# Kernel tuning notes

Hardware: AMD Instinct MI355X
Metric: run time of the kernel (lower is better)

## Reference

```python
import jax, jax.numpy as jnp
from jax import lax
import numpy as np

B, P, ENC, DEC, ATT, E, S, V = 32, 196, 512, 512, 512, 256, 128, 10000

def setup_inputs() -> dict:
    key = jax.random.key(0)
    ks = jax.random.split(key, 20)
    g = lambda k, shape, s=0.02: jax.random.normal(k, shape, dtype=jnp.float32) * s
    return {
        'features': jax.random.normal(ks[0], (B, P, ENC), dtype=jnp.float32),
        'captions': jax.random.randint(ks[1], (B, S), 0, V, dtype=jnp.int64),
        'emb': g(ks[2], (V, E)),
        'W_enc_att': g(ks[3], (ENC, ATT)), 'b_enc_att': jnp.zeros((ATT,), jnp.float32),
        'W_dec_att': g(ks[4], (DEC, ATT)), 'b_dec_att': jnp.zeros((ATT,), jnp.float32),
        'v_att': g(ks[5], (ATT,)), 'b_full_att': jnp.zeros((), jnp.float32),
        'W_init_h': g(ks[6], (ENC, DEC)), 'b_init_h': jnp.zeros((DEC,), jnp.float32),
        'W_init_c': g(ks[7], (ENC, DEC)), 'b_init_c': jnp.zeros((DEC,), jnp.float32),
        'W_ih': g(ks[8], (4 * DEC, E + ENC)), 'W_hh': g(ks[9], (4 * DEC, DEC)),
        'b_ih': jnp.zeros((4 * DEC,), jnp.float32), 'b_hh': jnp.zeros((4 * DEC,), jnp.float32),
        'W_fcn': g(ks[10], (DEC, V)), 'b_fcn': jnp.zeros((V,), jnp.float32),
    }

def reference(features, captions, emb, W_enc_att, b_enc_att, W_dec_att, b_dec_att,
              v_att, b_full_att, W_init_h, b_init_h, W_init_c, b_init_c,
              W_ih, W_hh, b_ih, b_hh, W_fcn, b_fcn):
    # init hidden state from mean encoder features
    mean_f = features.mean(axis=1)                    # [B, ENC]
    h = mean_f @ W_init_h + b_init_h                  # [B, DEC]
    c = mean_f @ W_init_c + b_init_c
    embeds = emb[captions]                            # [B, S, E]
    feat_proj = features @ W_enc_att + b_enc_att      # [B, P, ATT], loop-invariant

    def step(carry, emb_t):
        h, c = carry
        # additive attention: tanh(Uf + Wh) . v -> softmax -> weighted sum
        att = jnp.tanh(feat_proj + (h @ W_dec_att + b_dec_att)[:, None, :])  # [B, P, ATT]
        scores = att @ v_att + b_full_att             # [B, P]
        alpha = jax.nn.softmax(scores, axis=1)
        context = jnp.einsum('bp,bpe->be', alpha, features)  # [B, ENC]
        x = jnp.concatenate([emb_t, context], axis=1)  # [B, E+ENC]
        gates = x @ W_ih.T + b_ih + h @ W_hh.T + b_hh  # [B, 4*DEC]
        i, f, g, o = jnp.split(gates, 4, axis=1)
        c_new = jax.nn.sigmoid(f) * c + jax.nn.sigmoid(i) * jnp.tanh(g)
        h_new = jax.nn.sigmoid(o) * jnp.tanh(c_new)
        out = h_new @ W_fcn + b_fcn                    # dropout = identity (eval)
        return (h_new, c_new), out

    xs = jnp.swapaxes(embeds[:, :S - 1], 0, 1)         # [S-1, B, E]
    _, preds = lax.scan(step, (h, c), xs)              # [S-1, B, V]
    return jnp.swapaxes(preds, 0, 1)                   # [B, S-1, V]
```

## Files before the change

kernel.cpp:

```cpp
#include <hip/hip_runtime.h>
#include <hip/hip_bf16.h>
#include <stdint.h>

#define BB 32
#define PP 196
#define ENC 512
#define DEC 512
#define ATTD 512
#define EE 256
#define SS 128
#define VV 10000
#define TT 127
#define NBLK 512

typedef unsigned short ushort_t;
typedef unsigned int uint_t;
typedef unsigned long long u64_t;
typedef float f32x4 __attribute__((ext_vector_type(4)));
typedef short s16x8 __attribute__((ext_vector_type(8)));

__device__ __forceinline__ float bf2f(ushort_t u) {
    uint_t x = ((uint_t)u) << 16;
    return __uint_as_float(x);
}
__device__ __forceinline__ float bflo(uint_t u) { return __uint_as_float(u << 16); }
__device__ __forceinline__ float bfhi(uint_t u) { return __uint_as_float(u & 0xffff0000u); }
__device__ __forceinline__ ushort_t f2bf(float f) {
    uint_t u = __float_as_uint(f);
    uint_t r = (u + 0x7FFFu + ((u >> 16) & 1u)) >> 16;
    return (ushort_t)r;
}
__device__ __forceinline__ float ftanh(float x) {
    x = fminf(15.f, fmaxf(-15.f, x));
    float e = __expf(2.f * x);
    return (e - 1.f) * __builtin_amdgcn_rcpf(e + 1.f);
}
__device__ __forceinline__ float fsig(float x) {
    return __builtin_amdgcn_rcpf(1.f + __expf(-x));
}

__device__ __forceinline__ float aload1(const float* p) {
    return __hip_atomic_load(p, __ATOMIC_RELAXED, __HIP_MEMORY_SCOPE_AGENT);
}
__device__ __forceinline__ void astore1(float* p, float v) {
    __hip_atomic_store(p, v, __ATOMIC_RELAXED, __HIP_MEMORY_SCOPE_AGENT);
}
__device__ __forceinline__ float2 aload2(const float* p) {
    u64_t v = __hip_atomic_load((const u64_t*)p, __ATOMIC_RELAXED, __HIP_MEMORY_SCOPE_AGENT);
    float2 r;
    r.x = __uint_as_float((uint_t)v);
    r.y = __uint_as_float((uint_t)(v >> 32));
    return r;
}


__global__ void k_cvt(const float* __restrict__ s, ushort_t* __restrict__ d, int n) {
    for (int i = blockIdx.x * blockDim.x + threadIdx.x; i < n; i += gridDim.x * blockDim.x)
        d[i] = f2bf(s[i]);
}

__global__ void k_cvtD(const float* __restrict__ Wdec, ushort_t* __restrict__ out) {
    const int n = DEC * ATTD;
    for (int i = blockIdx.x * blockDim.x + threadIdx.x; i < n; i += gridDim.x * blockDim.x) {
        int k = i & (ATTD - 1);
        int j = i >> 9;
        out[i] = f2bf(Wdec[(size_t)k * ATTD + j]);
    }
}

__global__ void k_embed_bf(const int* __restrict__ cap, const float* __restrict__ emb,
                           ushort_t* __restrict__ out) {
    const int n = TT * BB * EE;
    for (int i = blockIdx.x * blockDim.x + threadIdx.x; i < n; i += gridDim.x * blockDim.x) {
        int e = i & (EE - 1);
        int b = (i >> 8) & (BB - 1);
        int t = i >> 13;
        int tok = cap[b * SS + t];
        out[i] = f2bf(emb[(size_t)tok * EE + e]);
    }
}

__global__ void k_cvtT(const float* __restrict__ Wih, ushort_t* __restrict__ out) {
    const int n = EE * 4 * DEC;
    for (int i = blockIdx.x * blockDim.x + threadIdx.x; i < n; i += gridDim.x * blockDim.x) {
        int k = i & (EE - 1);
        int row = i >> 8;
        out[(size_t)k * (4 * DEC) + row] = f2bf(Wih[(size_t)row * (EE + ENC) + k]);
    }
}

__global__ void k_cvtG2(const float* __restrict__ Wih, const float* __restrict__ Whh,
                        ushort_t* __restrict__ out) {
    const int n = 16 * 2 * 64 * 128 * 8;
    for (int i = blockIdx.x * blockDim.x + threadIdx.x; i < n; i += gridDim.x * blockDim.x) {
        int j = i & 7;
        int R = (i >> 3) & 127;
        int kc = (i >> 10) & 63;
        int kh = (i >> 16) & 1;
        int pcg = i >> 17;
        int d = pcg * 32 + (R >> 2);
        int gate = R & 3;
        int row = gate * DEC + d;
        int k = kh * 512 + kc * 8 + j;
        float v = (k < 512) ? Wih[(size_t)row * (EE + ENC) + EE + k]
                            : Whh[(size_t)row * DEC + (k - 512)];
        out[i] = f2bf(v);
    }
}

__global__ void k_bsum(const float* __restrict__ a, const float* __restrict__ b,
                       float* __restrict__ o, int n) {
    int i = blockIdx.x * blockDim.x + threadIdx.x;
    if (i < n) o[i] = a[i] + b[i];
}

__global__ __launch_bounds__(256) void k_init(const float* __restrict__ feat,
                                              const float* __restrict__ Wh, const float* __restrict__ bh,
                                              const float* __restrict__ Wc, const float* __restrict__ bc,
                                              float* __restrict__ h0, float* __restrict__ c0,
                                              int* __restrict__ bar) {
    __shared__ float ms[ENC];
    int b = blockIdx.x, t = threadIdx.x;
    if (b == 0) {
        for (int i = t; i < 4096; i += 256) bar[i] = 0;
    }
    for (int c = t; c < ENC; c += 256) {
        float s = 0.f;
        for (int p = 0; p < PP; ++p) s += feat[((size_t)b * PP + p) * ENC + c];
        ms[c] = s * (1.f / (float)PP);
    }
    __syncthreads();
    int d0 = 2 * t;
    float ah0 = 0.f, ah1 = 0.f, ac0 = 0.f, ac1 = 0.f;
    for (int k = 0; k < ENC; ++k) {
        float mk = ms[k];
        float2 wh = *(const float2*)(Wh + (size_t)k * DEC + d0);
        float2 wc = *(const float2*)(Wc + (size_t)k * DEC + d0);
        ah0 += mk * wh.x; ah1 += mk * wh.y;
        ac0 += mk * wc.x; ac1 += mk * wc.y;
    }
    h0[b * DEC + d0] = ah0 + bh[d0];
    h0[b * DEC + d0 + 1] = ah1 + bh[d0 + 1];
    c0[b * DEC + d0] = ac0 + bc[d0];
    c0[b * DEC + d0 + 1] = ac1 + bc[d0 + 1];
}

template <int MODE>
__global__ __launch_bounds__(256) void k_gemm(const ushort_t* __restrict__ A,
                                              const ushort_t* __restrict__ Bm,
                                              const float* __restrict__ bias,
                                              ushort_t* __restrict__ outb,
                                              float* __restrict__ outf,
                                              int M, int N, int K) {
    __shared__ __align__(16) ushort_t As[128 * 32];
    __shared__ __align__(16) ushort_t Bs[128 * 32];

    const int tid = threadIdx.x;
    const int wid = tid >> 6, lane = tid & 63;
    const int wm = wid >> 1, wn = wid & 1;
    const int lr = lane & 15, lk = (lane >> 4) * 8;
    const int row0 = blockIdx.x * 128, col0 = blockIdx.y * 128;

    f32x4 acc[4][4];
#pragma unroll
    for (int i = 0; i < 4; ++i)
#pragma unroll
        for (int j = 0; j < 4; ++j) acc[i][j] = (f32x4){0.f, 0.f, 0.f, 0.f};

    for (int k0 = 0; k0 < K; k0 += 32) {
        {
            int r = tid >> 1, kk = (tid & 1) * 16;
            int gr = row0 + r;
            uint4 v0 = {0, 0, 0, 0}, v1 = {0, 0, 0, 0};
            if (gr < M) {
                const ushort_t* sp = A + (size_t)gr * K + k0 + kk;
                v0 = *(const uint4*)sp;
                v1 = *(const uint4*)(sp + 8);
            }
            *(uint4*)(As + r * 32 + kk) = v0;
            *(uint4*)(As + r * 32 + kk + 8) = v1;
        }
        {
            int kk = tid >> 3;
            int n = (tid & 7) * 16;
            const ushort_t* sp = Bm + (size_t)(k0 + kk) * N + col0 + n;
            ushort_t tmp[16];
            if (col0 + n + 16 <= N) {
                *(uint4*)tmp = *(const uint4*)sp;
                *(uint4*)(tmp + 8) = *(const uint4*)(sp + 8);
            } else {
#pragma unroll
                for (int j = 0; j < 16; ++j) {
                    int c = col0 + n + j;
                    tmp[j] = (c < N) ? sp[j] : (ushort_t)0;
                }
            }
#pragma unroll
            for (int j = 0; j < 16; ++j) Bs[(n + j) * 32 + kk] = tmp[j];
        }
        __syncthreads();
        s16x8 af[4], bfr[4];
#pragma unroll
        for (int i = 0; i < 4; ++i)
            af[i] = *(const s16x8*)(As + (wm * 64 + i * 16 + lr) * 32 + lk);
#pragma unroll
        for (int j = 0; j < 4; ++j)
            bfr[j] = *(const s16x8*)(Bs + (wn * 64 + j * 16 + lr) * 32 + lk);
#pragma unroll
        for (int i = 0; i < 4; ++i)
#pragma unroll
            for (int j = 0; j < 4; ++j)
                acc[i][j] = __builtin_amdgcn_mfma_f32_16x16x32_bf16(af[i], bfr[j], acc[i][j], 0, 0, 0);
        __syncthreads();
    }

    const int lrow = (lane >> 4) * 4;
#pragma unroll
    for (int i = 0; i < 4; ++i) {
#pragma unroll
        for (int j = 0; j < 4; ++j) {
            int gr0 = row0 + wm * 64 + i * 16 + lrow;
            int gc = col0 + wn * 64 + j * 16 + lr;
#pragma unroll
            for (int r = 0; r < 4; ++r) {
                int gr = gr0 + r;
                if (gr < M && gc < N) {
                    float v = acc[i][j][r] + bias[gc];
                    if (MODE == 0) {
                        outb[(size_t)gr * N + gc] = f2bf(v);
                    } else {
                        int t = gr >> 5, b = gr & 31;
                        outf[((size_t)(b * TT + t)) * VV + gc] = v;
                    }
                }
            }
        }
    }
}


__device__ __forceinline__ void gbar16(int* cnt, int target) {
    asm volatile("s_waitcnt vmcnt(0)" ::: "memory");
    __syncthreads();
    if (threadIdx.x == 0) {
        __hip_atomic_fetch_add(cnt, 1, __ATOMIC_RELAXED, __HIP_MEMORY_SCOPE_AGENT);
        while (__hip_atomic_load(cnt, __ATOMIC_RELAXED, __HIP_MEMORY_SCOPE_AGENT) < target)
            __builtin_amdgcn_s_sleep(1);
    }
    __syncthreads();
}

__global__ __launch_bounds__(256) void k_steps(
    const ushort_t* __restrict__ fp, const ushort_t* __restrict__ fb,
    const ushort_t* __restrict__ WdecT, const float* __restrict__ bdec,
    const float* __restrict__ vatt, const float* __restrict__ bfull,
    const ushort_t* __restrict__ Wg2, const ushort_t* __restrict__ gemb,
    float* __restrict__ hbuf, const float* __restrict__ cbuf,
    float* __restrict__ a_glob, float* __restrict__ ctxP, float* __restrict__ Sp,
    ushort_t* __restrict__ Hb, int* __restrict__ bar) {

    __shared__ __align__(16) float hs[8 * 68];
    __shared__ __align__(16) float asS[544];
    __shared__ __align__(16) float vsS[544];
    __shared__ __align__(16) float cs[512];
    __shared__ __align__(16) float pctx[4 * 520];
    __shared__ float ep[16];
    __shared__ float sS[1];

    const int bid = blockIdx.x, tid = threadIdx.x;
    const float bfull_r = bfull[0];

    const int q = bid & 7, r = bid >> 3;
    const int pcg = 2 * q + (r & 1);
    const int bA = r >> 1;
    int* grpcnt = bar + 576 + bA * 32;

    const int aj = tid >> 3, akh = tid & 7;
    const int j_abs = pcg * 32 + aj;
    const float bdec_r = bdec[j_abs];
    const int pl = tid >> 4, ks = tid & 15;
    const int cnt_b = (pcg < 4) ? 13 : 12;
    const int p0 = (pcg < 4) ? pcg * 13 : 52 + (pcg - 4) * 12;
    const int ps = tid >> 6, cg = tid & 63;
    const int R = tid >> 1, ckh = tid & 1;
    const int cd = pcg * 32 + (R >> 2);
    const int crow = (R & 3) * DEC + cd;
    const ushort_t* wgp = Wg2 + ((size_t)(pcg * 2 + ckh) * 64) * 1024 + R * 8;

    float creg = ((tid & 7) == 0) ? cbuf[bA * DEC + cd] : 0.f;

    {
        int k0 = tid, k1 = tid + 256;
        vsS[(k0 & 31) + (k0 >> 5) * 34] = vatt[k0];
        vsS[(k1 & 31) + (k1 >> 5) * 34] = vatt[k1];
    }
    __syncthreads();

    for (int st = 0; st < TT; ++st) {
        const float* h_in = hbuf + (size_t)(st & 1) * BB * DEC;
        float* h_out = hbuf + (size_t)((st + 1) & 1) * BB * DEC;
        const size_t trow = (size_t)st * BB + bA;

        {
            float2 hv = aload2(h_in + bA * DEC + 2 * tid);
            int k0 = 2 * tid;
            float* hrow = hs + (k0 >> 6) * 68 + (k0 & 63);
            hrow[0] = hv.x;
            hrow[1] = hv.y;
        }
        __syncthreads();
        {
            const ushort_t* wp = WdecT + (size_t)j_abs * 512 + akh * 64;
            const float* hp = hs + akh * 68;
            float acc = 0.f;
#pragma unroll
            for (int c = 0; c < 8; ++c) {
                uint4 wv = *(const uint4*)(wp + c * 8);
                f32x4 x0 = *(const f32x4*)(hp + c * 8);
                f32x4 x1 = *(const f32x4*)(hp + c * 8 + 4);
                acc += bflo(wv.x) * x0[0] + bfhi(wv.x) * x0[1]
                     + bflo(wv.y) * x0[2] + bfhi(wv.y) * x0[3]
                     + bflo(wv.z) * x1[0] + bfhi(wv.z) * x1[1]
                     + bflo(wv.w) * x1[2] + bfhi(wv.w) * x1[3];
            }
            acc += __shfl_xor(acc, 1);
            acc += __shfl_xor(acc, 2);
            acc += __shfl_xor(acc, 4);
            if (akh == 0) astore1(a_glob + bA * ATTD + j_abs, acc + bdec_r);
        }
        gbar16(grpcnt, 16 * (3 * st + 1));

        {
            float2 av = aload2(a_glob + bA * ATTD + 2 * tid);
            int k0 = 2 * tid;
            float* arow = asS + (k0 & 31) + (k0 >> 5) * 34;
            arow[0] = av.x;
            arow[1] = av.y;
        }
        __syncthreads();
        {
            float acc = 0.f;
            if (pl < cnt_b) {
                const int p = p0 + pl;
                const ushort_t* fr = fp + ((size_t)bA * PP + p) * ATTD + ks * 32;
                const float* ap = asS + ks * 34;
                const float* vp = vsS + ks * 34;
#pragma unroll
                for (int c2 = 0; c2 < 4; ++c2) {
                    uint4 fv = *(const uint4*)(fr + c2 * 8);
                    const int c = c2 * 8;
                    float2 a0 = *(const float2*)(ap + c),     a1 = *(const float2*)(ap + c + 2);
                    float2 a2 = *(const float2*)(ap + c + 4), a3 = *(const float2*)(ap + c + 6);
                    float2 v0 = *(const float2*)(vp + c),     v1 = *(const float2*)(vp + c + 2);
                    float2 v2 = *(const float2*)(vp + c + 4), v3 = *(const float2*)(vp + c + 6);
                    acc += ftanh(bflo(fv.x) + a0.x) * v0.x;
                    acc += ftanh(bfhi(fv.x) + a0.y) * v0.y;
                    acc += ftanh(bflo(fv.y) + a1.x) * v1.x;
                    acc += ftanh(bfhi(fv.y) + a1.y) * v1.y;
                    acc += ftanh(bflo(fv.z) + a2.x) * v2.x;
                    acc += ftanh(bfhi(fv.z) + a2.y) * v2.y;
                    acc += ftanh(bflo(fv.w) + a3.x) * v3.x;
                    acc += ftanh(bfhi(fv.w) + a3.y) * v3.y;
                }
            }
            acc += __shfl_xor(acc, 1);
            acc += __shfl_xor(acc, 2);
            acc += __shfl_xor(acc, 4);
            acc += __shfl_xor(acc, 8);
            if (ks == 0) ep[pl] = (pl < cnt_b) ? __expf(acc + bfull_r) : 0.f;
        }
        __syncthreads();
        if (tid < 16) {
            float v = ep[tid];
            v += __shfl_xor(v, 1);
            v += __shfl_xor(v, 2);
            v += __shfl_xor(v, 4);
            v += __shfl_xor(v, 8);
            if (tid == 0) astore1(Sp + bA * 16 + pcg, v);
        }
        {
            float a8[8];
#pragma unroll
            for (int i2 = 0; i2 < 8; ++i2) a8[i2] = 0.f;
            for (int p2 = ps; p2 < cnt_b; p2 += 4) {
                float e2 = ep[p2];
                uint4 fv = *(const uint4*)(fb + ((size_t)bA * PP + p0 + p2) * ENC + cg * 8);
                a8[0] += e2 * bflo(fv.x); a8[1] += e2 * bfhi(fv.x);
                a8[2] += e2 * bflo(fv.y); a8[3] += e2 * bfhi(fv.y);
                a8[4] += e2 * bflo(fv.z); a8[5] += e2 * bfhi(fv.z);
                a8[6] += e2 * bflo(fv.w); a8[7] += e2 * bfhi(fv.w);
            }
            float* pp = pctx + ps * 520 + cg * 8;
            *(f32x4*)pp = (f32x4){a8[0], a8[1], a8[2], a8[3]};
            *(f32x4*)(pp + 4) = (f32x4){a8[4], a8[5], a8[6], a8[7]};
        }
        __syncthreads();
        {
            int c0i = 2 * tid, c1i = 2 * tid + 1;
            float s0 = pctx[c0i] + pctx[520 + c0i] + pctx[1040 + c0i] + pctx[1560 + c0i];
            float s1 = pctx[c1i] + pctx[520 + c1i] + pctx[1040 + c1i] + pctx[1560 + c1i];
            float* cp = ctxP + ((size_t)bA * 16 + pcg) * 512;
            astore1(cp + c0i, s0);
            astore1(cp + c1i, s1);
        }
        gbar16(grpcnt, 16 * (3 * st + 2));

        {
            if (tid < 16) {
                float s = aload1(Sp + bA * 16 + tid);
                s += __shfl_xor(s, 1);
                s += __shfl_xor(s, 2);
                s += __shfl_xor(s, 4);
                s += __shfl_xor(s, 8);
                if (tid == 0) sS[0] = s;
            }
            __syncthreads();
            const float invS = __builtin_amdgcn_rcpf(sS[0]);
            float s0 = 0.f, s1 = 0.f;
            const float* cp = ctxP + (size_t)bA * 16 * 512 + 2 * tid;
#pragma unroll
            for (int sl = 0; sl < 16; ++sl) {
                float2 v = aload2(cp + sl * 512);
                s0 += v.x;
                s1 += v.y;
            }
            cs[2 * tid] = s0 * invS;
            cs[2 * tid + 1] = s1 * invS;
        }
        __syncthreads();
        {
            float acc0 = 0.f, acc1 = 0.f;
#pragma unroll 8
            for (int kc = 0; kc < 64; ++kc) {
                uint4 wv = *(const uint4*)(wgp + kc * 1024);
                const float* xp = ckh ? (hs + (kc >> 3) * 68 + (kc & 7) * 8) : (cs + kc * 8);
                f32x4 x0 = *(const f32x4*)xp;
                f32x4 x1 = *(const f32x4*)(xp + 4);
                acc0 += bflo(wv.x) * x0[0] + bfhi(wv.x) * x0[1]
                      + bflo(wv.y) * x0[2] + bfhi(wv.y) * x0[3];
                acc1 += bflo(wv.z) * x1[0] + bfhi(wv.z) * x1[1]
                      + bflo(wv.w) * x1[2] + bfhi(wv.w) * x1[3];
            }
            float acc = acc0 + acc1;
            acc += __shfl_xor(acc, 1);
            const size_t gidx = trow * (4 * DEC) + crow;
            acc += bf2f(gemb[gidx]);
            float pf = __shfl_xor(acc, 2);
            float pg = __shfl_xor(acc, 4);
            float po = __shfl_xor(acc, 6);
            if ((tid & 7) == 0) {
                float cn = fsig(pf) * creg + fsig(acc) * ftanh(pg);
                float hn = fsig(po) * ftanh(cn);
                creg = cn;
                astore1(h_out + bA * DEC + cd, hn);
                Hb[trow * DEC + cd] = f2bf(hn);
            }
        }
        gbar16(grpcnt, 16 * (3 * st + 3));
    }
}


extern "C" void kernel_launch(void* const* d_in, const int* in_sizes, int n_in,
                              void* d_out, int out_size, void* d_ws, size_t ws_size,
                              hipStream_t stream) {
    const float* features  = (const float*)d_in[0];
    const int*   captions  = (const int*)d_in[1];
    const float* emb       = (const float*)d_in[2];
    const float* W_enc_att = (const float*)d_in[3];
    const float* b_enc_att = (const float*)d_in[4];
    const float* W_dec_att = (const float*)d_in[5];
    const float* b_dec_att = (const float*)d_in[6];
    const float* v_att     = (const float*)d_in[7];
    const float* b_full    = (const float*)d_in[8];
    const float* W_init_h  = (const float*)d_in[9];
    const float* b_init_h  = (const float*)d_in[10];
    const float* W_init_c  = (const float*)d_in[11];
    const float* b_init_c  = (const float*)d_in[12];
    const float* W_ih      = (const float*)d_in[13];
    const float* W_hh      = (const float*)d_in[14];
    const float* b_ih      = (const float*)d_in[15];
    const float* b_hh      = (const float*)d_in[16];
    const float* W_fcn     = (const float*)d_in[17];
    const float* b_fcn     = (const float*)d_in[18];
    float* out = (float*)d_out;
    char* ws = (char*)d_ws;

    size_t o = 0;
    ushort_t* Wfcn_b  = (ushort_t*)(ws + o); o += (size_t)DEC * VV * 2;
    ushort_t* Wenc_b  = (ushort_t*)(ws + o); o += (size_t)ENC * ATTD * 2;
    ushort_t* WdecT   = (ushort_t*)(ws + o); o += (size_t)DEC * ATTD * 2;
    ushort_t* fb      = (ushort_t*)(ws + o); o += (size_t)BB * PP * ENC * 2;
    ushort_t* fp_b    = (ushort_t*)(ws + o); o += (size_t)BB * PP * ATTD * 2;
    ushort_t* emb_bf  = (ushort_t*)(ws + o); o += (size_t)TT * BB * EE * 2;
    ushort_t* WihT    = (ushort_t*)(ws + o); o += (size_t)EE * 4 * DEC * 2;
    ushort_t* gembuf  = (ushort_t*)(ws + o); o += (size_t)TT * BB * 4 * DEC * 2;
    ushort_t* Wg2     = (ushort_t*)(ws + o); o += (size_t)4 * DEC * 1024 * 2;
    float*    bsum    = (float*)(ws + o);    o += (size_t)4 * DEC * 4;
    ushort_t* Hb      = (ushort_t*)(ws + o); o += (size_t)TT * BB * DEC * 2;
    float*    hbuf    = (float*)(ws + o);    o += (size_t)2 * BB * DEC * 4;
    float*    cbuf    = (float*)(ws + o);    o += (size_t)BB * DEC * 4;
    float*    a_glob  = (float*)(ws + o);    o += (size_t)BB * ATTD * 4;
    float*    ctxP    = (float*)(ws + o);    o += (size_t)BB * 16 * 512 * 4;
    float*    Sp      = (float*)(ws + o);    o += (size_t)BB * 16 * 4 + 64;
    int*      bar     = (int*)(ws + o);      o += 4096 * 4;

    k_cvt<<<2048, 256, 0, stream>>>(W_fcn, Wfcn_b, DEC * VV);
    k_cvt<<<256, 256, 0, stream>>>(W_enc_att, Wenc_b, ENC * ATTD);
    k_cvtD<<<256, 256, 0, stream>>>(W_dec_att, WdecT);
    k_cvt<<<2048, 256, 0, stream>>>(features, fb, BB * PP * ENC);
    k_embed_bf<<<1024, 256, 0, stream>>>(captions, emb, emb_bf);
    k_cvtT<<<1024, 256, 0, stream>>>(W_ih, WihT);
    k_cvtG2<<<4096, 256, 0, stream>>>(W_ih, W_hh, Wg2);
    k_bsum<<<8, 256, 0, stream>>>(b_ih, b_hh, bsum, 4 * DEC);
    k_init<<<32, 256, 0, stream>>>(features, W_init_h, b_init_h, W_init_c, b_init_c,
                                   hbuf, cbuf, bar);
    k_gemm<0><<<dim3((BB * PP) / 128, ATTD / 128), 256, 0, stream>>>(
        fb, Wenc_b, b_enc_att, fp_b, nullptr, BB * PP, ATTD, ENC);
    k_gemm<0><<<dim3((TT * BB + 127) / 128, (4 * DEC) / 128), 256, 0, stream>>>(
        emb_bf, WihT, bsum, gembuf, nullptr, TT * BB, 4 * DEC, EE);

    k_steps<<<NBLK, 256, 0, stream>>>(fp_b, fb, WdecT, b_dec_att, v_att, b_full,
                                      Wg2, gembuf, hbuf, cbuf,
                                      a_glob, ctxP, Sp, Hb, bar);

    k_gemm<1><<<dim3((TT * BB + 127) / 128, (VV + 127) / 128), 256, 0, stream>>>(
        Hb, Wfcn_b, b_fcn, nullptr, out, TT * BB, VV, DEC);
}
```

Baseline: 2.675 ms.

## Fuse decoder attention projection into LSTM update to drop one group barrier per step

Each block now computes a partial of the next step's h@W_dec_att, using the 32 hidden values it has just produced. It writes that partial to a per-slice buffer (paP), which is zero-initialized in k_init. At the start of the next step, the 16 partials are summed along with the bias. This removes the separate attention-projection phase and one of the three inter-block barriers per timestep. In exchange, each step reads 16 partial vectors from global memory, and the workspace grows by the size of the partial buffer.

```diff
diff --git a/kernel.cpp b/kernel.cpp
--- a/kernel.cpp
+++ b/kernel.cpp
@@ -118,12 +118,13 @@
                                               const float* __restrict__ Wh, const float* __restrict__ bh,
                                               const float* __restrict__ Wc, const float* __restrict__ bc,
                                               float* __restrict__ h0, float* __restrict__ c0,
-                                              int* __restrict__ bar) {
+                                              float* __restrict__ paP, int* __restrict__ bar) {
     __shared__ float ms[ENC];
     int b = blockIdx.x, t = threadIdx.x;
     if (b == 0) {
         for (int i = t; i < 4096; i += 256) bar[i] = 0;
     }
+    for (int i = t; i < 16 * 512; i += 256) paP[(size_t)b * 16 * 512 + i] = 0.f;
     for (int c = t; c < ENC; c += 256) {
         float s = 0.f;
         for (int p = 0; p < PP; ++p) s += feat[((size_t)b * PP + p) * ENC + c];
@@ -256,7 +257,7 @@
     const float* __restrict__ vatt, const float* __restrict__ bfull,
     const ushort_t* __restrict__ Wg2, const ushort_t* __restrict__ gemb,
     float* __restrict__ hbuf, const float* __restrict__ cbuf,
-    float* __restrict__ a_glob, float* __restrict__ ctxP, float* __restrict__ Sp,
+    float* __restrict__ paP, float* __restrict__ ctxP, float* __restrict__ Sp,
     ushort_t* __restrict__ Hb, int* __restrict__ bar) {
 
     __shared__ __align__(16) float hs[8 * 68];
@@ -264,6 +265,7 @@
     __shared__ __align__(16) float vsS[544];
     __shared__ __align__(16) float cs[512];
     __shared__ __align__(16) float pctx[4 * 520];
+    __shared__ __align__(16) float hsNew[32];
     __shared__ float ep[16];
     __shared__ float sS[1];
 
@@ -277,7 +279,6 @@
 
     const int aj = tid >> 3, akh = tid & 7;
     const int j_abs = pcg * 32 + aj;
-    const float bdec_r = bdec[j_abs];
     const int pl = tid >> 4, ks = tid & 15;
     const int cnt_b = (pcg < 4) ? 13 : 12;
     const int p0 = (pcg < 4) ? pcg * 13 : 52 + (pcg - 4) * 12;
@@ -286,6 +287,8 @@
     const int cd = pcg * 32 + (R >> 2);
     const int crow = (R & 3) * DEC + cd;
     const ushort_t* wgp = Wg2 + ((size_t)(pcg * 2 + ckh) * 64) * 1024 + R * 8;
+    float* mypa = paP + ((size_t)bA * 16 + pcg) * 512;
+    const float2 bdec2 = *(const float2*)(bdec + 2 * tid);
 
     float creg = ((tid & 7) == 0) ? cbuf[bA * DEC + cd] : 0.f;
 
@@ -296,46 +299,55 @@
     }
     __syncthreads();
 
+    {
+        float2 hv = aload2(hbuf + bA * DEC + 2 * tid);
+        int k0 = 2 * tid;
+        float* hrow = hs + (k0 >> 6) * 68 + (k0 & 63);
+        hrow[0] = hv.x;
+        hrow[1] = hv.y;
+        __syncthreads();
+        const ushort_t* wp = WdecT + (size_t)j_abs * 512 + akh * 64;
+        const float* hp = hs + akh * 68;
+        float acc = 0.f;
+#pragma unroll
+        for (int c = 0; c < 8; ++c) {
+            uint4 wv = *(const uint4*)(wp + c * 8);
+            f32x4 x0 = *(const f32x4*)(hp + c * 8);
+            f32x4 x1 = *(const f32x4*)(hp + c * 8 + 4);
+            acc += bflo(wv.x) * x0[0] + bfhi(wv.x) * x0[1]
+                 + bflo(wv.y) * x0[2] + bfhi(wv.y) * x0[3]
+                 + bflo(wv.z) * x1[0] + bfhi(wv.z) * x1[1]
+                 + bflo(wv.w) * x1[2] + bfhi(wv.w) * x1[3];
+        }
+        acc += __shfl_xor(acc, 1);
+        acc += __shfl_xor(acc, 2);
+        acc += __shfl_xor(acc, 4);
+        if (akh == 0) astore1(mypa + j_abs, acc);
+    }
+    gbar16(grpcnt, 16);
+
     for (int st = 0; st < TT; ++st) {
         const float* h_in = hbuf + (size_t)(st & 1) * BB * DEC;
         float* h_out = hbuf + (size_t)((st + 1) & 1) * BB * DEC;
         const size_t trow = (size_t)st * BB + bA;
 
         {
+            float s0 = bdec2.x, s1 = bdec2.y;
+            const float* pap = paP + (size_t)bA * 16 * 512 + 2 * tid;
+#pragma unroll
+            for (int sl = 0; sl < 16; ++sl) {
+                float2 v = aload2(pap + sl * 512);
+                s0 += v.x;
+                s1 += v.y;
+            }
+            int k0 = 2 * tid;
+            float* arow = asS + (k0 & 31) + (k0 >> 5) * 34;
+            arow[0] = s0;
+            arow[1] = s1;
             float2 hv = aload2(h_in + bA * DEC + 2 * tid);
-            int k0 = 2 * tid;
             float* hrow = hs + (k0 >> 6) * 68 + (k0 & 63);
             hrow[0] = hv.x;
             hrow[1] = hv.y;
-        }
-        __syncthreads();
-        {
-            const ushort_t* wp = WdecT + (size_t)j_abs * 512 + akh * 64;
-            const float* hp = hs + akh * 68;
-            float acc = 0.f;
-#pragma unroll
-            for (int c = 0; c < 8; ++c) {
-                uint4 wv = *(const uint4*)(wp + c * 8);
-                f32x4 x0 = *(const f32x4*)(hp + c * 8);
-                f32x4 x1 = *(const f32x4*)(hp + c * 8 + 4);
-                acc += bflo(wv.x) * x0[0] + bfhi(wv.x) * x0[1]
-                     + bflo(wv.y) * x0[2] + bfhi(wv.y) * x0[3]
-                     + bflo(wv.z) * x1[0] + bfhi(wv.z) * x1[1]
-                     + bflo(wv.w) * x1[2] + bfhi(wv.w) * x1[3];
-            }
-            acc += __shfl_xor(acc, 1);
-            acc += __shfl_xor(acc, 2);
-            acc += __shfl_xor(acc, 4);
-            if (akh == 0) astore1(a_glob + bA * ATTD + j_abs, acc + bdec_r);
-        }
-        gbar16(grpcnt, 16 * (3 * st + 1));
-
-        {
-            float2 av = aload2(a_glob + bA * ATTD + 2 * tid);
-            int k0 = 2 * tid;
-            float* arow = asS + (k0 & 31) + (k0 >> 5) * 34;
-            arow[0] = av.x;
-            arow[1] = av.y;
         }
         __syncthreads();
         {
@@ -403,7 +415,7 @@
             astore1(cp + c0i, s0);
             astore1(cp + c1i, s1);
         }
-        gbar16(grpcnt, 16 * (3 * st + 2));
+        gbar16(grpcnt, 16 * (2 * st + 2));
 
         {
             if (tid < 16) {
@@ -454,9 +466,33 @@
                 creg = cn;
                 astore1(h_out + bA * DEC + cd, hn);
                 Hb[trow * DEC + cd] = f2bf(hn);
-            }
-        }
-        gbar16(grpcnt, 16 * (3 * st + 3));
+                hsNew[tid >> 3] = hn;
+            }
+        }
+        __syncthreads();
+        {
+            const int j0 = 2 * tid;
+            const ushort_t* w0 = WdecT + (size_t)j0 * 512 + pcg * 32;
+            const ushort_t* w1 = w0 + 512;
+            float pa0 = 0.f, pa1 = 0.f;
+#pragma unroll
+            for (int c = 0; c < 4; ++c) {
+                uint4 wv0 = *(const uint4*)(w0 + c * 8);
+                uint4 wv1 = *(const uint4*)(w1 + c * 8);
+                const float* hp = hsNew + c * 8;
+                pa0 += bflo(wv0.x) * hp[0] + bfhi(wv0.x) * hp[1]
+                     + bflo(wv0.y) * hp[2] + bfhi(wv0.y) * hp[3]
+                     + bflo(wv0.z) * hp[4] + bfhi(wv0.z) * hp[5]
+                     + bflo(wv0.w) * hp[6] + bfhi(wv0.w) * hp[7];
+                pa1 += bflo(wv1.x) * hp[0] + bfhi(wv1.x) * hp[1]
+                     + bflo(wv1.y) * hp[2] + bfhi(wv1.y) * hp[3]
+                     + bflo(wv1.z) * hp[4] + bfhi(wv1.z) * hp[5]
+                     + bflo(wv1.w) * hp[6] + bfhi(wv1.w) * hp[7];
+            }
+            astore1(mypa + j0, pa0);
+            astore1(mypa + j0 + 1, pa1);
+        }
+        gbar16(grpcnt, 16 * (2 * st + 3));
     }
 }
 
@@ -500,7 +536,7 @@
     ushort_t* Hb      = (ushort_t*)(ws + o); o += (size_t)TT * BB * DEC * 2;
     float*    hbuf    = (float*)(ws + o);    o += (size_t)2 * BB * DEC * 4;
     float*    cbuf    = (float*)(ws + o);    o += (size_t)BB * DEC * 4;
-    float*    a_glob  = (float*)(ws + o);    o += (size_t)BB * ATTD * 4;
+    float*    paP     = (float*)(ws + o);    o += (size_t)BB * 16 * 512 * 4;
     float*    ctxP    = (float*)(ws + o);    o += (size_t)BB * 16 * 512 * 4;
     float*    Sp      = (float*)(ws + o);    o += (size_t)BB * 16 * 4 + 64;
     int*      bar     = (int*)(ws + o);      o += 4096 * 4;
@@ -514,7 +550,7 @@
     k_cvtG2<<<4096, 256, 0, stream>>>(W_ih, W_hh, Wg2);
     k_bsum<<<8, 256, 0, stream>>>(b_ih, b_hh, bsum, 4 * DEC);
     k_init<<<32, 256, 0, stream>>>(features, W_init_h, b_init_h, W_init_c, b_init_c,
-                                   hbuf, cbuf, bar);
+                                   hbuf, cbuf, paP, bar);
     k_gemm<0><<<dim3((BB * PP) / 128, ATTD / 128), 256, 0, stream>>>(
         fb, Wenc_b, b_enc_att, fp_b, nullptr, BB * PP, ATTD, ENC);
     k_gemm<0><<<dim3((TT * BB + 127) / 128, (4 * DEC) / 128), 256, 0, stream>>>(
@@ -522,7 +558,7 @@
 
     k_steps<<<NBLK, 256, 0, stream>>>(fp_b, fb, WdecT, b_dec_att, v_att, b_full,
                                       Wg2, gembuf, hbuf, cbuf,
-                                      a_glob, ctxP, Sp, Hb, bar);
+                                      paP, ctxP, Sp, Hb, bar);
 
     k_gemm<1><<<dim3((TT * BB + 127) / 128, (VV + 127) / 128), 256, 0, stream>>>(
         Hb, Wfcn_b, b_fcn, nullptr, out, TT * BB, VV, DEC);
```

Result: slower. 2.899 ms (+8.4%).

## Precompute features×W_ih_ctx so per-step context matvec becomes gate-space weighted sum

Applied to the files above, without the earlier changes.

Uses associativity to precompute G = features @ W_ih_ctx^T, shape [B*P, 2048], with one upfront GEMM. Each recurrent step then forms gate contributions directly as an alpha-weighted sum over G, removing the per-step context reduction and the 512-wide context matvec. The W_hh matvec is hoisted before the barrier so it overlaps the attention phase, and partial sums travel as bf16 through global memory. In exchange, each step reads a 4x wider per-pixel row (2048 vs 512), adds a large precomputed buffer, and rounds partials to bf16, which costs precision.

```diff
diff --git a/kernel.cpp b/kernel.cpp
--- a/kernel.cpp
+++ b/kernel.cpp
@@ -12,6 +12,7 @@
 #define VV 10000
 #define TT 127
 #define NBLK 512
+#define NR 2048
 
 typedef unsigned short ushort_t;
 typedef unsigned int uint_t;
@@ -51,6 +52,12 @@
     r.x = __uint_as_float((uint_t)v);
     r.y = __uint_as_float((uint_t)(v >> 32));
     return r;
+}
+__device__ __forceinline__ u64_t aload8(const ushort_t* p) {
+    return __hip_atomic_load((const u64_t*)p, __ATOMIC_RELAXED, __HIP_MEMORY_SCOPE_AGENT);
+}
+__device__ __forceinline__ void astore_h(ushort_t* p, ushort_t v) {
+    __hip_atomic_store(p, v, __ATOMIC_RELAXED, __HIP_MEMORY_SCOPE_AGENT);
 }
 
 
@@ -89,22 +96,26 @@
     }
 }
 
-__global__ void k_cvtG2(const float* __restrict__ Wih, const float* __restrict__ Whh,
-                        ushort_t* __restrict__ out) {
-    const int n = 16 * 2 * 64 * 128 * 8;
+__global__ void k_cvtX(const float* __restrict__ Wih, ushort_t* __restrict__ out) {
+    const int n = 512 * NR;
+    for (int i = blockIdx.x * blockDim.x + threadIdx.x; i < n; i += gridDim.x * blockDim.x) {
+        int row = i & (NR - 1);
+        int k = i >> 11;
+        out[i] = f2bf(Wih[(size_t)row * (EE + ENC) + EE + k]);
+    }
+}
+
+__global__ void k_cvtH(const float* __restrict__ Whh, ushort_t* __restrict__ out) {
+    const int n = 16 * 2 * 32 * 128 * 8;
     for (int i = blockIdx.x * blockDim.x + threadIdx.x; i < n; i += gridDim.x * blockDim.x) {
         int j = i & 7;
         int R = (i >> 3) & 127;
-        int kc = (i >> 10) & 63;
-        int kh = (i >> 16) & 1;
-        int pcg = i >> 17;
-        int d = pcg * 32 + (R >> 2);
-        int gate = R & 3;
-        int row = gate * DEC + d;
-        int k = kh * 512 + kc * 8 + j;
-        float v = (k < 512) ? Wih[(size_t)row * (EE + ENC) + EE + k]
-                            : Whh[(size_t)row * DEC + (k - 512)];
-        out[i] = f2bf(v);
+        int kc = (i >> 10) & 31;
+        int kh = (i >> 15) & 1;
+        int pcg = i >> 16;
+        int row = (R & 3) * DEC + pcg * 32 + (R >> 2);
+        int k = kh * 256 + kc * 8 + j;
+        out[i] = f2bf(Whh[(size_t)row * DEC + k]);
     }
 }
 
@@ -112,6 +123,11 @@
                        float* __restrict__ o, int n) {
     int i = blockIdx.x * blockDim.x + threadIdx.x;
     if (i < n) o[i] = a[i] + b[i];
+}
+
+__global__ void k_zerof(float* __restrict__ o, int n) {
+    int i = blockIdx.x * blockDim.x + threadIdx.x;
+    if (i < n) o[i] = 0.f;
 }
 
 __global__ __launch_bounds__(256) void k_init(const float* __restrict__ feat,
@@ -251,19 +267,18 @@
 }
 
 __global__ __launch_bounds__(256) void k_steps(
-    const ushort_t* __restrict__ fp, const ushort_t* __restrict__ fb,
+    const ushort_t* __restrict__ fp,
     const ushort_t* __restrict__ WdecT, const float* __restrict__ bdec,
     const float* __restrict__ vatt, const float* __restrict__ bfull,
-    const ushort_t* __restrict__ Wg2, const ushort_t* __restrict__ gemb,
+    const ushort_t* __restrict__ Wh3, const ushort_t* __restrict__ G,
+    const ushort_t* __restrict__ gemb,
     float* __restrict__ hbuf, const float* __restrict__ cbuf,
-    float* __restrict__ a_glob, float* __restrict__ ctxP, float* __restrict__ Sp,
+    float* __restrict__ a_glob, ushort_t* __restrict__ P, float* __restrict__ Sp,
     ushort_t* __restrict__ Hb, int* __restrict__ bar) {
 
     __shared__ __align__(16) float hs[8 * 68];
     __shared__ __align__(16) float asS[544];
     __shared__ __align__(16) float vsS[544];
-    __shared__ __align__(16) float cs[512];
-    __shared__ __align__(16) float pctx[4 * 520];
     __shared__ float ep[16];
     __shared__ float sS[1];
 
@@ -281,11 +296,11 @@
     const int pl = tid >> 4, ks = tid & 15;
     const int cnt_b = (pcg < 4) ? 13 : 12;
     const int p0 = (pcg < 4) ? pcg * 13 : 52 + (pcg - 4) * 12;
-    const int ps = tid >> 6, cg = tid & 63;
+    const int rowc = tid * 8;
     const int R = tid >> 1, ckh = tid & 1;
     const int cd = pcg * 32 + (R >> 2);
     const int crow = (R & 3) * DEC + cd;
-    const ushort_t* wgp = Wg2 + ((size_t)(pcg * 2 + ckh) * 64) * 1024 + R * 8;
+    const ushort_t* whp = Wh3 + ((size_t)(pcg * 2 + ckh) * 32) * 1024 + R * 8;
 
     float creg = ((tid & 7) == 0) ? cbuf[bA * DEC + cd] : 0.f;
 
@@ -295,6 +310,8 @@
         vsS[(k1 & 31) + (k1 >> 5) * 34] = vatt[k1];
     }
     __syncthreads();
+
+    float acc_hh = 0.f;
 
     for (int st = 0; st < TT; ++st) {
         const float* h_in = hbuf + (size_t)(st & 1) * BB * DEC;
@@ -379,29 +396,36 @@
             if (tid == 0) astore1(Sp + bA * 16 + pcg, v);
         }
         {
+            acc_hh = 0.f;
+#pragma unroll 8
+            for (int kc = 0; kc < 32; ++kc) {
+                uint4 wv = *(const uint4*)(whp + kc * 1024);
+                int k0 = ckh * 256 + kc * 8;
+                const float* xp = hs + (k0 >> 6) * 68 + (k0 & 63);
+                f32x4 x0 = *(const f32x4*)xp;
+                f32x4 x1 = *(const f32x4*)(xp + 4);
+                acc_hh += bflo(wv.x) * x0[0] + bfhi(wv.x) * x0[1]
+                        + bflo(wv.y) * x0[2] + bfhi(wv.y) * x0[3]
+                        + bflo(wv.z) * x1[0] + bfhi(wv.z) * x1[1]
+                        + bflo(wv.w) * x1[2] + bfhi(wv.w) * x1[3];
+            }
+        }
+        {
             float a8[8];
 #pragma unroll
             for (int i2 = 0; i2 < 8; ++i2) a8[i2] = 0.f;
-            for (int p2 = ps; p2 < cnt_b; p2 += 4) {
+            const ushort_t* gp = G + ((size_t)(bA * PP + p0)) * NR + rowc;
+            for (int p2 = 0; p2 < cnt_b; ++p2) {
                 float e2 = ep[p2];
-                uint4 fv = *(const uint4*)(fb + ((size_t)bA * PP + p0 + p2) * ENC + cg * 8);
-                a8[0] += e2 * bflo(fv.x); a8[1] += e2 * bfhi(fv.x);
-                a8[2] += e2 * bflo(fv.y); a8[3] += e2 * bfhi(fv.y);
-                a8[4] += e2 * bflo(fv.z); a8[5] += e2 * bfhi(fv.z);
-                a8[6] += e2 * bflo(fv.w); a8[7] += e2 * bfhi(fv.w);
-            }
-            float* pp = pctx + ps * 520 + cg * 8;
-            *(f32x4*)pp = (f32x4){a8[0], a8[1], a8[2], a8[3]};
-            *(f32x4*)(pp + 4) = (f32x4){a8[4], a8[5], a8[6], a8[7]};
-        }
-        __syncthreads();
-        {
-            int c0i = 2 * tid, c1i = 2 * tid + 1;
-            float s0 = pctx[c0i] + pctx[520 + c0i] + pctx[1040 + c0i] + pctx[1560 + c0i];
-            float s1 = pctx[c1i] + pctx[520 + c1i] + pctx[1040 + c1i] + pctx[1560 + c1i];
-            float* cp = ctxP + ((size_t)bA * 16 + pcg) * 512;
-            astore1(cp + c0i, s0);
-            astore1(cp + c1i, s1);
+                uint4 gv = *(const uint4*)(gp + (size_t)p2 * NR);
+                a8[0] += e2 * bflo(gv.x); a8[1] += e2 * bfhi(gv.x);
+                a8[2] += e2 * bflo(gv.y); a8[3] += e2 * bfhi(gv.y);
+                a8[4] += e2 * bflo(gv.z); a8[5] += e2 * bfhi(gv.z);
+                a8[6] += e2 * bflo(gv.w); a8[7] += e2 * bfhi(gv.w);
+            }
+            ushort_t* pp = P + ((size_t)bA * NR + rowc) * 16 + pcg;
+#pragma unroll
+            for (int j2 = 0; j2 < 8; ++j2) astore_h(pp + j2 * 16, f2bf(a8[j2]));
         }
         gbar16(grpcnt, 16 * (3 * st + 2));
 
@@ -415,36 +439,27 @@
                 if (tid == 0) sS[0] = s;
             }
             __syncthreads();
-            const float invS = __builtin_amdgcn_rcpf(sS[0]);
-            float s0 = 0.f, s1 = 0.f;
-            const float* cp = ctxP + (size_t)bA * 16 * 512 + 2 * tid;
-#pragma unroll
-            for (int sl = 0; sl < 16; ++sl) {
-                float2 v = aload2(cp + sl * 512);
-                s0 += v.x;
-                s1 += v.y;
-            }
-            cs[2 * tid] = s0 * invS;
-            cs[2 * tid + 1] = s1 * invS;
-        }
-        __syncthreads();
-        {
-            float acc0 = 0.f, acc1 = 0.f;
-#pragma unroll 8
-            for (int kc = 0; kc < 64; ++kc) {
-                uint4 wv = *(const uint4*)(wgp + kc * 1024);
-                const float* xp = ckh ? (hs + (kc >> 3) * 68 + (kc & 7) * 8) : (cs + kc * 8);
-                f32x4 x0 = *(const f32x4*)xp;
-                f32x4 x1 = *(const f32x4*)(xp + 4);
-                acc0 += bflo(wv.x) * x0[0] + bfhi(wv.x) * x0[1]
-                      + bflo(wv.y) * x0[2] + bfhi(wv.y) * x0[3];
-                acc1 += bflo(wv.z) * x1[0] + bfhi(wv.z) * x1[1]
-                      + bflo(wv.w) * x1[2] + bfhi(wv.w) * x1[3];
-            }
-            float acc = acc0 + acc1;
-            acc += __shfl_xor(acc, 1);
-            const size_t gidx = trow * (4 * DEC) + crow;
-            acc += bf2f(gemb[gidx]);
+            float gn = 0.f;
+            if (ckh == 0) {
+                const ushort_t* pp = P + ((size_t)bA * NR + crow) * 16;
+                u64_t w0 = aload8(pp);
+                u64_t w1 = aload8(pp + 4);
+                u64_t w2 = aload8(pp + 8);
+                u64_t w3 = aload8(pp + 12);
+                float s = 0.f;
+#pragma unroll
+                for (int j2 = 0; j2 < 4; ++j2) s += bf2f((ushort_t)(w0 >> (16 * j2)));
+#pragma unroll
+                for (int j2 = 0; j2 < 4; ++j2) s += bf2f((ushort_t)(w1 >> (16 * j2)));
+#pragma unroll
+                for (int j2 = 0; j2 < 4; ++j2) s += bf2f((ushort_t)(w2 >> (16 * j2)));
+#pragma unroll
+                for (int j2 = 0; j2 < 4; ++j2) s += bf2f((ushort_t)(w3 >> (16 * j2)));
+                gn = s * __builtin_amdgcn_rcpf(sS[0]);
+            }
+            float accp = gn + acc_hh;
+            float acc = accp + __shfl_xor(accp, 1);
+            acc += bf2f(gemb[trow * (4 * DEC) + crow]);
             float pf = __shfl_xor(acc, 2);
             float pg = __shfl_xor(acc, 4);
             float po = __shfl_xor(acc, 6);
@@ -495,13 +510,16 @@
     ushort_t* emb_bf  = (ushort_t*)(ws + o); o += (size_t)TT * BB * EE * 2;
     ushort_t* WihT    = (ushort_t*)(ws + o); o += (size_t)EE * 4 * DEC * 2;
     ushort_t* gembuf  = (ushort_t*)(ws + o); o += (size_t)TT * BB * 4 * DEC * 2;
-    ushort_t* Wg2     = (ushort_t*)(ws + o); o += (size_t)4 * DEC * 1024 * 2;
+    ushort_t* WctxT   = (ushort_t*)(ws + o); o += (size_t)512 * NR * 2;
+    ushort_t* Wh3     = (ushort_t*)(ws + o); o += (size_t)16 * 2 * 32 * 128 * 8 * 2;
+    ushort_t* G       = (ushort_t*)(ws + o); o += (size_t)BB * PP * NR * 2;
     float*    bsum    = (float*)(ws + o);    o += (size_t)4 * DEC * 4;
+    float*    zb      = (float*)(ws + o);    o += (size_t)NR * 4;
     ushort_t* Hb      = (ushort_t*)(ws + o); o += (size_t)TT * BB * DEC * 2;
     float*    hbuf    = (float*)(ws + o);    o += (size_t)2 * BB * DEC * 4;
     float*    cbuf    = (float*)(ws + o);    o += (size_t)BB * DEC * 4;
     float*    a_glob  = (float*)(ws + o);    o += (size_t)BB * ATTD * 4;
-    float*    ctxP    = (float*)(ws + o);    o += (size_t)BB * 16 * 512 * 4;
+    ushort_t* P       = (ushort_t*)(ws + o); o += (size_t)BB * NR * 16 * 2;
     float*    Sp      = (float*)(ws + o);    o += (size_t)BB * 16 * 4 + 64;
     int*      bar     = (int*)(ws + o);      o += 4096 * 4;
 
@@ -511,18 +529,22 @@
     k_cvt<<<2048, 256, 0, stream>>>(features, fb, BB * PP * ENC);
     k_embed_bf<<<1024, 256, 0, stream>>>(captions, emb, emb_bf);
     k_cvtT<<<1024, 256, 0, stream>>>(W_ih, WihT);
-    k_cvtG2<<<4096, 256, 0, stream>>>(W_ih, W_hh, Wg2);
+    k_cvtX<<<1024, 256, 0, stream>>>(W_ih, WctxT);
+    k_cvtH<<<1024, 256, 0, stream>>>(W_hh, Wh3);
     k_bsum<<<8, 256, 0, stream>>>(b_ih, b_hh, bsum, 4 * DEC);
+    k_zerof<<<8, 256, 0, stream>>>(zb, NR);
     k_init<<<32, 256, 0, stream>>>(features, W_init_h, b_init_h, W_init_c, b_init_c,
                                    hbuf, cbuf, bar);
     k_gemm<0><<<dim3((BB * PP) / 128, ATTD / 128), 256, 0, stream>>>(
         fb, Wenc_b, b_enc_att, fp_b, nullptr, BB * PP, ATTD, ENC);
     k_gemm<0><<<dim3((TT * BB + 127) / 128, (4 * DEC) / 128), 256, 0, stream>>>(
         emb_bf, WihT, bsum, gembuf, nullptr, TT * BB, 4 * DEC, EE);
-
-    k_steps<<<NBLK, 256, 0, stream>>>(fp_b, fb, WdecT, b_dec_att, v_att, b_full,
-                                      Wg2, gembuf, hbuf, cbuf,
-                                      a_glob, ctxP, Sp, Hb, bar);
+    k_gemm<0><<<dim3((BB * PP) / 128, NR / 128), 256, 0, stream>>>(
+        fb, WctxT, zb, G, nullptr, BB * PP, NR, ENC);
+
+    k_steps<<<NBLK, 256, 0, stream>>>(fp_b, WdecT, b_dec_att, v_att, b_full,
+                                      Wh3, G, gembuf, hbuf, cbuf,
+                                      a_glob, P, Sp, Hb, bar);
 
     k_gemm<1><<<dim3((TT * BB + 127) / 128, (VV + 127) / 128), 256, 0, stream>>>(
         Hb, Wfcn_b, b_fcn, nullptr, out, TT * BB, VV, DEC);
```

Result: slower. 3.832 ms (+43.3%).
